# Kernel optimization log

Hardware: AMD Instinct MI355X
Metric: run time of the kernel (lower is better)

The kernel has to match this reference:

```python
import jax, jax.numpy as jnp
import numpy as np

D_IN = 768
D_LATENT = 16384
BATCH = 8192
K = 32


def _xavier(key, shape):
    fan_out, fan_in = shape
    limit = float(np.sqrt(6.0 / (fan_in + fan_out)))
    return jax.random.uniform(key, shape, jnp.float32, -limit, limit)


def setup_inputs() -> dict:
    key = jax.random.key(0)
    k1, k2, k3 = jax.random.split(key, 3)
    x = jax.random.normal(k1, (BATCH, D_IN), dtype=jnp.float32)
    W_enc = _xavier(k2, (D_LATENT, D_IN))   # encoder.weight: [d_latent, d_in]
    W_dec = _xavier(k3, (D_IN, D_LATENT))   # decoder.weight: [d_in, d_latent]
    return {"x": x, "W_enc": W_enc, "W_dec": W_dec, "k": K}


def reference(x, W_enc, W_dec, k):
    # Encoder: Linear (no bias) + ReLU -> z: [B, d_latent]
    z = jax.nn.relu(jnp.einsum('bd,ld->bl', x, W_enc))
    # Per-row top-k mask via scatter of ones at top-k indices
    _, idx = jax.lax.top_k(z, k)                      # idx: [B, k]
    rows = jnp.arange(z.shape[0])[:, None]            # [B, 1]
    mask = jnp.zeros_like(z).at[rows, idx].set(1.0)
    z = z * mask
    # Decoder: Linear (no bias) -> x_hat: [B, d_in]
    x_hat = jnp.einsum('bl,dl->bd', z, W_dec)
    return x_hat, z
```

## Files before the change

kernel.cpp:

```cpp
#include <hip/hip_runtime.h>
#include <hip/hip_bf16.h>
#include <stdint.h>

#define MB 8192
#define NL 16384
#define KD 768
#define TOPK 32
#define CAND_NEED 48
#define TAU 0.70f
#define CAP_MIN 288

typedef short bf16x8 __attribute__((ext_vector_type(8)));
typedef float f32x4 __attribute__((ext_vector_type(4)));
typedef float f32x2 __attribute__((ext_vector_type(2)));
typedef unsigned short ushort_t;

__device__ __forceinline__ short f2bf(float f) {
  unsigned u = __builtin_bit_cast(unsigned, f);
  u = (u + 0x7fffu + ((u >> 16) & 1u)) >> 16;
  return (short)u;
}
__device__ __forceinline__ float bf2f(ushort_t u) {
  return __builtin_bit_cast(float, (unsigned)u << 16);
}

__device__ __forceinline__ void gload16(const ushort_t* g, short* l) {
  __builtin_amdgcn_global_load_lds(
      (const __attribute__((address_space(1))) void*)g,
      (__attribute__((address_space(3))) void*)l, 16, 0, 0);
}

__global__ __launch_bounds__(256) void cvt_bf16(const float* __restrict__ in,
                                                ushort_t* __restrict__ out, int n8,
                                                int* __restrict__ cnt0) {
  int i = blockIdx.x * 256 + threadIdx.x;
  if (cnt0 && blockIdx.x < 32) cnt0[blockIdx.x * 256 + threadIdx.x] = 0;
  if (i >= n8) return;
  const float4 v0 = *(const float4*)(in + (size_t)i * 8);
  const float4 v1 = *(const float4*)(in + (size_t)i * 8 + 4);
  bf16x8 p;
  p[0] = f2bf(v0.x); p[1] = f2bf(v0.y); p[2] = f2bf(v0.z); p[3] = f2bf(v0.w);
  p[4] = f2bf(v1.x); p[5] = f2bf(v1.y); p[6] = f2bf(v1.z); p[7] = f2bf(v1.w);
  *(bf16x8*)(out + (size_t)i * 8) = p;
}

__global__ __launch_bounds__(256) void transpose_wdec(const float* __restrict__ W,
                                                      ushort_t* __restrict__ WT) {
  __shared__ float tile[32][33];
  int l0 = blockIdx.x * 32;
  int d0 = blockIdx.y * 32;
  int lx = threadIdx.x;
  for (int i = threadIdx.y; i < 32; i += 8)
    tile[i][lx] = W[(size_t)(d0 + i) * NL + (l0 + lx)];
  __syncthreads();
  for (int i = threadIdx.y; i < 32; i += 8)
    WT[(size_t)(l0 + i) * KD + (d0 + lx)] = (ushort_t)f2bf(tile[lx][i]);
}

#define GBM 128
#define GBN 128
#define GBK 32
#define LDA 32

__device__ __forceinline__ void emit_cands(const f32x4 (&acc)[4][4], int m0, int n0,
                                           int wr64, int wc64, int er, int ec,
                                           int* __restrict__ cnt,
                                           unsigned* __restrict__ lists, int cap) {
#pragma unroll
  for (int i = 0; i < 4; i++)
#pragma unroll
    for (int j = 0; j < 4; j++)
#pragma unroll
      for (int r = 0; r < 4; r++) {
        float v = acc[i][j][r];
        if (v > TAU) {
          int grow = m0 + wr64 + i * 16 + er + r;
          int gcol = n0 + wc64 + j * 16 + ec;
          int pos = atomicAdd(&cnt[grow], 1);
          if (pos < cap)
            lists[(size_t)grow * cap + pos] =
                (unsigned)gcol | ((unsigned)(ushort_t)f2bf(v) << 16);
        }
      }
}

__global__ __launch_bounds__(256, 4) void encoder_gemm_pre2(const ushort_t* __restrict__ Xb,
                                                            const ushort_t* __restrict__ Wb,
                                                            int* __restrict__ cnt,
                                                            unsigned* __restrict__ lists,
                                                            int cap) {
  __shared__ short Al[2][GBM][LDA];
  __shared__ short Bl[2][GBN][LDA];

  const int tid = threadIdx.x;
  const int NBN = NL / GBN;
  const int GROUP = 8;
  const int NWG = (MB / GBM) * NBN;
  const int CPX = NWG / 8;
  int bid = (blockIdx.x % 8) * CPX + blockIdx.x / 8;
  int group = bid / (GROUP * NBN);
  int rem = bid % (GROUP * NBN);
  int bm = group * GROUP + (rem % GROUP);
  int bn = rem / GROUP;
  const int m0 = bm * GBM, n0 = bn * GBN;

  const int srow = tid >> 2;
  const int slog = (tid & 3) ^ ((tid >> 3) & 3);
  const int w = tid >> 6;

  const ushort_t* Asrc = Xb + (size_t)(m0 + srow) * KD + slog * 8;
  const ushort_t* Bsrc = Wb + (size_t)(n0 + srow) * KD + slog * 8;

#define STAGE(BUF, KT)                                              \
  {                                                                 \
    const int koff_ = (KT) * GBK;                                   \
    short* la_ = &Al[BUF][0][0] + w * 512;                          \
    short* lb_ = &Bl[BUF][0][0] + w * 512;                          \
    gload16(Asrc + koff_, la_);                                     \
    gload16(Asrc + (size_t)64 * KD + koff_, la_ + 2048);            \
    gload16(Bsrc + koff_, lb_);                                     \
    gload16(Bsrc + (size_t)64 * KD + koff_, lb_ + 2048);            \
  }

  const int lane = tid & 63;
  const int wr64 = (w >> 1) * 64;
  const int wc64 = (w & 1) * 64;
  const int fr = lane & 15;
  const int fkb_sw = (((lane >> 4) ^ ((fr >> 1) & 3))) * 8;

  f32x4 acc[4][4];
#pragma unroll
  for (int i = 0; i < 4; i++)
#pragma unroll
    for (int j = 0; j < 4; j++)
#pragma unroll
      for (int r = 0; r < 4; r++) acc[i][j][r] = 0.f;

  STAGE(0, 0);
  STAGE(1, 1);

  const int NT = KD / GBK;
  for (int kt = 0; kt < NT; kt++) {
    if (kt + 1 < NT) {
      asm volatile("s_waitcnt vmcnt(4)" ::: "memory");
    } else {
      asm volatile("s_waitcnt vmcnt(0)" ::: "memory");
    }
    __builtin_amdgcn_s_barrier();

    const int cur = kt & 1;
    bf16x8 af[4], bg[4];
#pragma unroll
    for (int i = 0; i < 4; i++)
      af[i] = *(const bf16x8*)&Al[cur][wr64 + i * 16 + fr][fkb_sw];
#pragma unroll
    for (int j = 0; j < 4; j++)
      bg[j] = *(const bf16x8*)&Bl[cur][wc64 + j * 16 + fr][fkb_sw];

#pragma unroll
    for (int i = 0; i < 4; i++)
#pragma unroll
      for (int j = 0; j < 4; j++)
        acc[i][j] = __builtin_amdgcn_mfma_f32_16x16x32_bf16(af[i], bg[j], acc[i][j], 0, 0, 0);

    __builtin_amdgcn_s_barrier();
    if (kt + 2 < NT) STAGE(cur, kt + 2);
  }

  const int er = (lane >> 4) * 4;
  const int ec = lane & 15;
  emit_cands(acc, m0, n0, wr64, wc64, er, ec, cnt, lists, cap);
#undef STAGE
}

__global__ __launch_bounds__(256, 4) void encoder_gemm_f32(const float* __restrict__ X,
                                                           const float* __restrict__ Wenc,
                                                           int* __restrict__ cnt,
                                                           unsigned* __restrict__ lists,
                                                           int cap) {
  __shared__ short Al[2][GBM][LDA];
  __shared__ short Bl[2][GBN][LDA];

  const int tid = threadIdx.x;
  const int NBN = NL / GBN;
  const int GROUP = 8;
  int bid = blockIdx.x;
  int group = bid / (GROUP * NBN);
  int rem = bid % (GROUP * NBN);
  int bm = group * GROUP + (rem % GROUP);
  int bn = rem / GROUP;
  const int m0 = bm * GBM, n0 = bn * GBN;

  const int srow = tid >> 2;
  const int skg = tid & 3;
  const int sw8 = (skg ^ ((srow >> 1) & 3)) * 8;

  const float* Abase = X + (size_t)(m0 + srow) * KD + skg * 8;
  const float* Bbase = Wenc + (size_t)(n0 + srow) * KD + skg * 8;

  float4 ra0, ra1, ra2, ra3, rb0, rb1, rb2, rb3;

#define FLOADS(KT)                                         \
  {                                                        \
    const float* ap_ = Abase + (KT) * GBK;                 \
    const float* bp_ = Bbase + (KT) * GBK;                 \
    ra0 = *(const float4*)(ap_);                           \
    ra1 = *(const float4*)(ap_ + 4);                       \
    ra2 = *(const float4*)(ap_ + (size_t)64 * KD);         \
    ra3 = *(const float4*)(ap_ + (size_t)64 * KD + 4);     \
    rb0 = *(const float4*)(bp_);                           \
    rb1 = *(const float4*)(bp_ + 4);                       \
    rb2 = *(const float4*)(bp_ + (size_t)64 * KD);         \
    rb3 = *(const float4*)(bp_ + (size_t)64 * KD + 4);     \
  }

#define CVT8(DST, FA, FB)                                                    \
  {                                                                          \
    bf16x8 p_;                                                               \
    p_[0] = f2bf(FA.x); p_[1] = f2bf(FA.y); p_[2] = f2bf(FA.z);              \
    p_[3] = f2bf(FA.w); p_[4] = f2bf(FB.x); p_[5] = f2bf(FB.y);              \
    p_[6] = f2bf(FB.z); p_[7] = f2bf(FB.w);                                  \
    *(bf16x8*)(DST) = p_;                                                    \
  }

#define FWRITE(BUF)                                      \
  {                                                      \
    CVT8(&Al[BUF][srow][sw8], ra0, ra1);                 \
    CVT8(&Al[BUF][srow + 64][sw8], ra2, ra3);            \
    CVT8(&Bl[BUF][srow][sw8], rb0, rb1);                 \
    CVT8(&Bl[BUF][srow + 64][sw8], rb2, rb3);            \
  }

  const int lane = tid & 63;
  const int w = tid >> 6;
  const int wr64 = (w >> 1) * 64;
  const int wc64 = (w & 1) * 64;
  const int fr = lane & 15;
  const int fkb_sw = (((lane >> 4) ^ ((fr >> 1) & 3))) * 8;

  f32x4 acc[4][4];
#pragma unroll
  for (int i = 0; i < 4; i++)
#pragma unroll
    for (int j = 0; j < 4; j++)
#pragma unroll
      for (int r = 0; r < 4; r++) acc[i][j][r] = 0.f;

  FLOADS(0);
  FWRITE(0);
  __syncthreads();

  const int NT = KD / GBK;
  for (int kt = 0; kt < NT; kt++) {
    const int cur = kt & 1;
    if (kt + 1 < NT) FLOADS(kt + 1);

    bf16x8 af[4], bg[4];
#pragma unroll
    for (int i = 0; i < 4; i++)
      af[i] = *(const bf16x8*)&Al[cur][wr64 + i * 16 + fr][fkb_sw];
#pragma unroll
    for (int j = 0; j < 4; j++)
      bg[j] = *(const bf16x8*)&Bl[cur][wc64 + j * 16 + fr][fkb_sw];

#pragma unroll
    for (int i = 0; i < 4; i++)
#pragma unroll
      for (int j = 0; j < 4; j++)
        acc[i][j] = __builtin_amdgcn_mfma_f32_16x16x32_bf16(af[i], bg[j], acc[i][j], 0, 0, 0);

    if (kt + 1 < NT) FWRITE(cur ^ 1);
    __syncthreads();
  }

  const int er = (lane >> 4) * 4;
  const int ec = lane & 15;
  emit_cands(acc, m0, n0, wr64, wc64, er, ec, cnt, lists, cap);
#undef FLOADS
#undef CVT8
#undef FWRITE
}

__global__ __launch_bounds__(256) void select_decode(const int* __restrict__ cnt,
                                                     const unsigned* __restrict__ lists,
                                                     int cap,
                                                     const float* __restrict__ X,
                                                     const float* __restrict__ Wenc,
                                                     const ushort_t* __restrict__ WdTb,
                                                     const float* __restrict__ Wdec,
                                                     int use_wdt,
                                                     float* __restrict__ Z,
                                                     float* __restrict__ Xhat) {
  __shared__ float xrow[4][KD];
  __shared__ unsigned keys[4][512];
  __shared__ int s48_j[4][CAND_NEED];
  __shared__ float s48_v[4][CAND_NEED];
  __shared__ int sel_j[4][TOPK];
  __shared__ float sel_v[4][TOPK];

  const int tid = threadIdx.x;
  const int w = tid >> 6;
  const int lane = tid & 63;
  const int row = blockIdx.x * 4 + w;
  float* z = Z + (size_t)row * NL;

  {
    const float4* xs = (const float4*)(X + (size_t)row * KD);
    float4* xd = (float4*)xrow[w];
#pragma unroll
    for (int q = 0; q < 3; q++) xd[lane + 64 * q] = xs[lane + 64 * q];
  }

  const int n = cnt[row];
  const bool fb = (n < CAND_NEED) || (n > cap) || (n > 512);

  if (!fb) {
    for (int i = lane; i < n; i += 64)
      keys[w][i] = lists[(size_t)row * cap + i] ^ 0xFFFFu;
    for (int i = lane; i < n; i += 64) {
      unsigned ki = keys[w][i];
      int r = 0;
      for (int c = 0; c < n; c++) r += (int)(keys[w][c] > ki);
      if (r < CAND_NEED) s48_j[w][r] = (int)((~ki) & 0xFFFFu);
    }
    if (lane < CAND_NEED) {
      const float4* wr4 = (const float4*)(Wenc + (size_t)s48_j[w][lane] * KD);
      float s = 0.f;
#pragma unroll 8
      for (int k4 = 0; k4 < KD / 4; k4++) {
        float4 wv = wr4[k4];
        s = fmaf(xrow[w][4 * k4 + 0], wv.x, s);
        s = fmaf(xrow[w][4 * k4 + 1], wv.y, s);
        s = fmaf(xrow[w][4 * k4 + 2], wv.z, s);
        s = fmaf(xrow[w][4 * k4 + 3], wv.w, s);
      }
      s48_v[w][lane] = s;
    }
    {
      const f32x4 zf = {0.f, 0.f, 0.f, 0.f};
      f32x4* z4 = (f32x4*)z;
      for (int i = lane; i < NL / 4; i += 64)
        __builtin_nontemporal_store(zf, z4 + i);
    }
    if (lane < CAND_NEED) {
      float vi = s48_v[w][lane];
      int ji = s48_j[w][lane];
      int r = 0;
      for (int c = 0; c < CAND_NEED; c++) {
        float vc = s48_v[w][c];
        r += (int)((vc > vi) || (vc == vi && s48_j[w][c] < ji));
      }
      if (r < TOPK) { sel_j[w][r] = ji; sel_v[w][r] = fmaxf(vi, 0.f); }
    }
    asm volatile("s_waitcnt vmcnt(0)" ::: "memory");
    if (lane < TOPK) z[sel_j[w][lane]] = sel_v[w][lane];
  } else {
    for (int j = lane; j < NL; j += 64) {
      const float* wr = Wenc + (size_t)j * KD;
      float s = 0.f;
      for (int k = 0; k < KD; k++) s = fmaf(xrow[w][k], wr[k], s);
      z[j] = fmaxf(s, 0.f);
    }
    asm volatile("s_waitcnt vmcnt(0)" ::: "memory");
    for (int t = 0; t < TOPK; t++) {
      float bm = -1.f;
      int bi = NL;
      for (int j = lane; j < NL; j += 64) {
        float v = z[j];
        if (v > bm || (v == bm && j < bi)) { bm = v; bi = j; }
      }
#pragma unroll
      for (int off = 32; off > 0; off >>= 1) {
        float vo = __shfl_down(bm, off);
        int io = __shfl_down(bi, off);
        if (vo > bm || (vo == bm && io < bi)) { bm = vo; bi = io; }
      }
      bm = __shfl(bm, 0);
      bi = __shfl(bi, 0);
      if (lane == 0) {
        sel_j[w][t] = bi;
        sel_v[w][t] = bm;
        z[bi] = -1.f;
      }
      asm volatile("s_waitcnt vmcnt(0)" ::: "memory");
    }
    for (int j = lane; j < NL; j += 64) z[j] = 0.f;
    asm volatile("s_waitcnt vmcnt(0)" ::: "memory");
    if (lane < TOPK) z[sel_j[w][lane]] = sel_v[w][lane];
  }

  float alo[6], ahi[6];
#pragma unroll
  for (int q = 0; q < 6; q++) { alo[q] = 0.f; ahi[q] = 0.f; }
  if (use_wdt) {
    for (int t = 0; t < TOPK; t++) {
      float v = sel_v[w][t];
      const unsigned* wr = (const unsigned*)(WdTb + (size_t)sel_j[w][t] * KD);
#pragma unroll
      for (int q = 0; q < 6; q++) {
        unsigned u = wr[q * 64 + lane];
        alo[q] = fmaf(v, bf2f((ushort_t)(u & 0xffffu)), alo[q]);
        ahi[q] = fmaf(v, bf2f((ushort_t)(u >> 16)), ahi[q]);
      }
    }
  } else {
    for (int t = 0; t < TOPK; t++) {
      float v = sel_v[w][t];
      const float* wc = Wdec + sel_j[w][t];
#pragma unroll
      for (int q = 0; q < 6; q++) {
        int d = q * 128 + lane * 2;
        alo[q] = fmaf(v, wc[(size_t)d * NL], alo[q]);
        ahi[q] = fmaf(v, wc[(size_t)(d + 1) * NL], ahi[q]);
      }
    }
  }
  float* xo = Xhat + (size_t)row * KD;
#pragma unroll
  for (int q = 0; q < 6; q++) {
    f32x2 st = {alo[q], ahi[q]};
    __builtin_nontemporal_store(st, (f32x2*)(xo + q * 128 + lane * 2));
  }
}

extern "C" void kernel_launch(void* const* d_in, const int* in_sizes, int n_in,
                              void* d_out, int out_size, void* d_ws, size_t ws_size,
                              hipStream_t stream) {
  const float* x = (const float*)d_in[0];
  const float* Wenc = (const float*)d_in[1];
  const float* Wdec = (const float*)d_in[2];

  float* xhat = (float*)d_out;
  float* z = (float*)d_out + (size_t)MB * KD;

  const size_t cnt_b = (size_t)MB * sizeof(int);
  const size_t wsh_b = (size_t)NL * KD * sizeof(ushort_t);
  const size_t xb_b = (size_t)MB * KD * sizeof(ushort_t);
  const size_t entry = sizeof(unsigned);

  char* ws = (char*)d_ws;
  int* cnt = (int*)ws;
  size_t off = cnt_b;

  int use_pre = 0, use_wdt = 0, cap = 1;
  ushort_t* Wsh = nullptr;
  ushort_t* Xb = nullptr;
  unsigned* lists = nullptr;

  if (ws_size >= cnt_b + wsh_b + xb_b + (size_t)MB * entry * CAP_MIN) {
    use_pre = 1; use_wdt = 1;
    Wsh = (ushort_t*)(ws + off); off += wsh_b;
    Xb = (ushort_t*)(ws + off); off += xb_b;
    lists = (unsigned*)(ws + off);
    size_t c = (ws_size - off) / ((size_t)MB * entry);
    cap = (int)(c > 512 ? 512 : c);
  } else if (ws_size >= cnt_b + wsh_b + (size_t)MB * entry * CAP_MIN) {
    use_wdt = 1;
    Wsh = (ushort_t*)(ws + off); off += wsh_b;
    lists = (unsigned*)(ws + off);
    size_t c = (ws_size - off) / ((size_t)MB * entry);
    cap = (int)(c > 512 ? 512 : c);
  } else {
    lists = (unsigned*)(ws + off);
    size_t avail = (ws_size > off) ? (ws_size - off) : 0;
    size_t c = avail / ((size_t)MB * entry);
    cap = (int)(c > 512 ? 512 : c);
    if (cap < 1) cap = 1;
  }

  if (use_pre) {
    int nx8 = MB * KD / 8, nw8 = NL * KD / 8;
    cvt_bf16<<<(nx8 + 255) / 256, 256, 0, stream>>>(x, Xb, nx8, cnt);
    cvt_bf16<<<(nw8 + 255) / 256, 256, 0, stream>>>(Wenc, Wsh, nw8, nullptr);
    encoder_gemm_pre2<<<(MB / GBM) * (NL / GBN), 256, 0, stream>>>(Xb, Wsh, cnt, lists, cap);
    dim3 g(NL / 32, KD / 32);
    transpose_wdec<<<g, dim3(32, 8), 0, stream>>>(Wdec, Wsh);
  } else {
    hipMemsetAsync(cnt, 0, cnt_b, stream);
    if (use_wdt) {
      dim3 g(NL / 32, KD / 32);
      transpose_wdec<<<g, dim3(32, 8), 0, stream>>>(Wdec, Wsh);
    }
    encoder_gemm_f32<<<(MB / GBM) * (NL / GBN), 256, 0, stream>>>(x, Wenc, cnt, lists, cap);
  }
  select_decode<<<MB / 4, 256, 0, stream>>>(cnt, lists, cap, x, Wenc, Wsh, Wdec, use_wdt,
                                            z, xhat);
}
```

Before: 628.0 us.

## Replace encoder GEMM with 256x256 tile, 8-wave kernel using dynamic LDS

```diff
diff --git a/kernel.cpp b/kernel.cpp
--- a/kernel.cpp
+++ b/kernel.cpp
@@ -84,93 +84,126 @@
       }
 }
 
-__global__ __launch_bounds__(256, 4) void encoder_gemm_pre2(const ushort_t* __restrict__ Xb,
-                                                            const ushort_t* __restrict__ Wb,
-                                                            int* __restrict__ cnt,
-                                                            unsigned* __restrict__ lists,
-                                                            int cap) {
-  __shared__ short Al[2][GBM][LDA];
-  __shared__ short Bl[2][GBN][LDA];
+#define QBM 256
+#define QBN 256
+#define QBK 64
+__global__ __launch_bounds__(512, 2) void encoder_gemm_8w(const ushort_t* __restrict__ Xb,
+                                                          const ushort_t* __restrict__ Wb,
+                                                          int* __restrict__ cnt,
+                                                          unsigned* __restrict__ lists,
+                                                          int cap) {
+  extern __shared__ short smem[];
+  short* As = smem;
+  short* Bs = smem + 32768;
 
   const int tid = threadIdx.x;
-  const int NBN = NL / GBN;
+  const int w = tid >> 6;
+  const int lane = tid & 63;
+
+  const int NBN = NL / QBN;
   const int GROUP = 8;
-  const int NWG = (MB / GBM) * NBN;
+  const int NWG = (MB / QBM) * NBN;
   const int CPX = NWG / 8;
   int bid = (blockIdx.x % 8) * CPX + blockIdx.x / 8;
   int group = bid / (GROUP * NBN);
   int rem = bid % (GROUP * NBN);
   int bm = group * GROUP + (rem % GROUP);
   int bn = rem / GROUP;
-  const int m0 = bm * GBM, n0 = bn * GBN;
+  const int m0 = bm * QBM, n0 = bn * QBN;
 
   const int srow = tid >> 2;
   const int slog = (tid & 3) ^ ((tid >> 3) & 3);
-  const int w = tid >> 6;
-
   const ushort_t* Asrc = Xb + (size_t)(m0 + srow) * KD + slog * 8;
   const ushort_t* Bsrc = Wb + (size_t)(n0 + srow) * KD + slog * 8;
 
-#define STAGE(BUF, KT)                                              \
-  {                                                                 \
-    const int koff_ = (KT) * GBK;                                   \
-    short* la_ = &Al[BUF][0][0] + w * 512;                          \
-    short* lb_ = &Bl[BUF][0][0] + w * 512;                          \
-    gload16(Asrc + koff_, la_);                                     \
-    gload16(Asrc + (size_t)64 * KD + koff_, la_ + 2048);            \
-    gload16(Bsrc + koff_, lb_);                                     \
-    gload16(Bsrc + (size_t)64 * KD + koff_, lb_ + 2048);            \
-  }
-
-  const int lane = tid & 63;
-  const int wr64 = (w >> 1) * 64;
-  const int wc64 = (w & 1) * 64;
+#define STAGEQ(BUF, KT)                                                     \
+  {                                                                         \
+    _Pragma("unroll")                                                       \
+    for (int sb = 0; sb < 2; sb++) {                                        \
+      const int ko_ = (KT) * QBK + sb * 32;                                 \
+      short* la_ = As + ((BUF) * 2 + sb) * 8192 + w * 512;                  \
+      short* lb_ = Bs + ((BUF) * 2 + sb) * 8192 + w * 512;                  \
+      gload16(Asrc + ko_, la_);                                             \
+      gload16(Asrc + (size_t)128 * KD + ko_, la_ + 4096);                   \
+      gload16(Bsrc + ko_, lb_);                                             \
+      gload16(Bsrc + (size_t)128 * KD + ko_, lb_ + 4096);                   \
+    }                                                                       \
+  }
+
+  const int wr = (w >> 2) * 128;
+  const int wc = (w & 3) * 64;
   const int fr = lane & 15;
-  const int fkb_sw = (((lane >> 4) ^ ((fr >> 1) & 3))) * 8;
-
-  f32x4 acc[4][4];
-#pragma unroll
-  for (int i = 0; i < 4; i++)
+  const int fkb = (((lane >> 4) ^ ((fr >> 1) & 3))) * 8;
+
+  f32x4 acc[8][4];
+#pragma unroll
+  for (int i = 0; i < 8; i++)
 #pragma unroll
     for (int j = 0; j < 4; j++)
 #pragma unroll
       for (int r = 0; r < 4; r++) acc[i][j][r] = 0.f;
 
-  STAGE(0, 0);
-  STAGE(1, 1);
-
-  const int NT = KD / GBK;
+  STAGEQ(0, 0)
+  STAGEQ(1, 1)
+
+  const int NT = KD / QBK;
   for (int kt = 0; kt < NT; kt++) {
     if (kt + 1 < NT) {
-      asm volatile("s_waitcnt vmcnt(4)" ::: "memory");
+      asm volatile("s_waitcnt vmcnt(8)" ::: "memory");
     } else {
       asm volatile("s_waitcnt vmcnt(0)" ::: "memory");
     }
     __builtin_amdgcn_s_barrier();
 
     const int cur = kt & 1;
-    bf16x8 af[4], bg[4];
-#pragma unroll
-    for (int i = 0; i < 4; i++)
-      af[i] = *(const bf16x8*)&Al[cur][wr64 + i * 16 + fr][fkb_sw];
-#pragma unroll
-    for (int j = 0; j < 4; j++)
-      bg[j] = *(const bf16x8*)&Bl[cur][wc64 + j * 16 + fr][fkb_sw];
-
-#pragma unroll
-    for (int i = 0; i < 4; i++)
+    bf16x8 af[8][2], bg[4][2];
+#pragma unroll
+    for (int sb = 0; sb < 2; sb++) {
+      const short* Ab = As + (cur * 2 + sb) * 8192;
+      const short* Bb = Bs + (cur * 2 + sb) * 8192;
+#pragma unroll
+      for (int i = 0; i < 8; i++)
+        af[i][sb] = *(const bf16x8*)(Ab + (wr + i * 16 + fr) * 32 + fkb);
 #pragma unroll
       for (int j = 0; j < 4; j++)
-        acc[i][j] = __builtin_amdgcn_mfma_f32_16x16x32_bf16(af[i], bg[j], acc[i][j], 0, 0, 0);
-
+        bg[j][sb] = *(const bf16x8*)(Bb + (wc + j * 16 + fr) * 32 + fkb);
+    }
+    asm volatile("s_waitcnt lgkmcnt(0)" ::: "memory");
+    __builtin_amdgcn_sched_barrier(0);
     __builtin_amdgcn_s_barrier();
-    if (kt + 2 < NT) STAGE(cur, kt + 2);
+    if (kt + 2 < NT) STAGEQ(cur, kt + 2)
+
+    __builtin_amdgcn_s_setprio(1);
+#pragma unroll
+    for (int sb = 0; sb < 2; sb++)
+#pragma unroll
+      for (int i = 0; i < 8; i++)
+#pragma unroll
+        for (int j = 0; j < 4; j++)
+          acc[i][j] = __builtin_amdgcn_mfma_f32_16x16x32_bf16(af[i][sb], bg[j][sb],
+                                                              acc[i][j], 0, 0, 0);
+    __builtin_amdgcn_s_setprio(0);
   }
 
   const int er = (lane >> 4) * 4;
   const int ec = lane & 15;
-  emit_cands(acc, m0, n0, wr64, wc64, er, ec, cnt, lists, cap);
-#undef STAGE
+#pragma unroll
+  for (int i = 0; i < 8; i++)
+#pragma unroll
+    for (int j = 0; j < 4; j++)
+#pragma unroll
+      for (int r = 0; r < 4; r++) {
+        float v = acc[i][j][r];
+        if (v > TAU) {
+          int grow = m0 + wr + i * 16 + er + r;
+          int gcol = n0 + wc + j * 16 + ec;
+          int pos = atomicAdd(&cnt[grow], 1);
+          if (pos < cap)
+            lists[(size_t)grow * cap + pos] =
+                (unsigned)gcol | ((unsigned)(ushort_t)f2bf(v) << 16);
+        }
+      }
+#undef STAGEQ
 }
 
 __global__ __launch_bounds__(256, 4) void encoder_gemm_f32(const float* __restrict__ X,
@@ -469,10 +502,17 @@
   }
 
   if (use_pre) {
+    static bool attr_set = false;
+    if (!attr_set) {
+      hipFuncSetAttribute((const void*)encoder_gemm_8w,
+                          hipFuncAttributeMaxDynamicSharedMemorySize, 131072);
+      attr_set = true;
+    }
     int nx8 = MB * KD / 8, nw8 = NL * KD / 8;
     cvt_bf16<<<(nx8 + 255) / 256, 256, 0, stream>>>(x, Xb, nx8, cnt);
     cvt_bf16<<<(nw8 + 255) / 256, 256, 0, stream>>>(Wenc, Wsh, nw8, nullptr);
-    encoder_gemm_pre2<<<(MB / GBM) * (NL / GBN), 256, 0, stream>>>(Xb, Wsh, cnt, lists, cap);
+    encoder_gemm_8w<<<(MB / QBM) * (NL / QBN), 512, 131072, stream>>>(Xb, Wsh, cnt,
+                                                                      lists, cap);
     dim3 g(NL / 32, KD / 32);
     transpose_wdec<<<g, dim3(32, 8), 0, stream>>>(Wdec, Wsh);
   } else {
```

After: 722.4 us. 1.15x slower.
